# Performance work log

Hardware: AMD Instinct MI355X
Metric: run time of the kernel (lower is better)

## Reference

```python
import jax, jax.numpy as jnp
import numpy as np
import jax.scipy.linalg as jsl

K = 4           # num_hops + 1
N = 4096        # nodes
D = 256         # in_dim == out_dim
S = 32          # subspace_dim
ETA = 0.5
EPS = 0.5


def setup_inputs() -> dict:
    key = jax.random.key(0)
    k1, k2, k3 = jax.random.split(key, 3)
    hops = jax.random.normal(k1, (K, N, D), dtype=jnp.float32)
    A = (jax.random.uniform(k2, (N, N)) < 0.01).astype(jnp.float32)
    A = jnp.maximum(A, A.T)
    A = jnp.fill_diagonal(A, 1.0, inplace=False)
    deg = A.sum(axis=1)
    L = jnp.diag(deg) - A  # graph Laplacian
    # orthonormal subspace bases via QR, as in __init__
    raw = jax.random.normal(k3, (K, D, S), dtype=jnp.float32)
    q, _ = jnp.linalg.qr(raw)
    U = q[:, :, :S]
    hop_weights = jnp.ones((K,), dtype=jnp.float32) / K
    threshold = jnp.full((D,), 0.05, dtype=jnp.float32)
    lambda_lap = jnp.asarray(0.1, dtype=jnp.float32)
    return {"hops": hops, "adj_mask": A, "L": L, "U": U,
            "hop_weights": hop_weights, "threshold": threshold,
            "lambda_lap": lambda_lap}


def reference(hops, adj_mask, L, U, hop_weights, threshold, lambda_lap):
    n = hops.shape[1]
    s = U.shape[-1]
    w = jax.nn.softmax(hop_weights, axis=0)
    mask_add = (1.0 - adj_mask) * -1e9  # [n, n]
    I_s = jnp.eye(s, dtype=hops.dtype)
    agg_total = jnp.zeros((hops.shape[2], n), dtype=hops.dtype)  # [d, n]
    coeff = s / (n * EPS ** 2)
    for k in range(K):  # small fixed hop count
        Uk = U[k]                      # [d, s]
        Zk = Uk.T @ hops[k].T          # [s, n]
        M_k = I_s + coeff * (Zk @ Zk.T)  # [s, s]
        cf = jsl.cho_factor(M_k)
        M_inv = jsl.cho_solve(cf, I_s)   # Cholesky inverse
        MZ = M_inv @ Zk                  # [s, n]
        scores = Zk.T @ MZ + mask_add    # [n, n] Mahalanobis-style attention
        alpha = jax.nn.softmax(scores, axis=1)
        grad_k = Uk @ (MZ @ alpha.T)     # [d, n]
        agg_total = agg_total + w[k] * grad_k
    H_agg = agg_total.T                  # [n, d]
    lap_grad = lambda_lap * (L @ H_agg)
    H_half = hops[0] + ETA * H_agg - ETA * lap_grad
    # soft-threshold (proximal step); in_dim == out_dim so no proj
    H_out = jnp.sign(H_half) * jax.nn.relu(jnp.abs(H_half) - threshold[None, :])
    # orthogonality regularizer over subspace bases
    orth_loss = jnp.asarray(0.0, dtype=hops.dtype)
    for k in range(K):
        UkTUk = U[k].T @ U[k]
        orth_loss = orth_loss + ((UkTUk - I_s) ** 2).sum()
        for l in range(k + 1, K):
            orth_loss = orth_loss + ((U[k].T @ U[l]) ** 2).sum()
    lap_smooth = jnp.sum(H_out * (L @ H_out))  # trace(H^T L H)
    return (H_out, orth_loss, lap_smooth, jax.lax.stop_gradient(w))
```

## Files before the change

kernel.cpp:

```cpp
#include <hip/hip_runtime.h>
#include <cstddef>

typedef unsigned short ushortt;
typedef unsigned int uintt;

static constexpr int Nn = 4096;
static constexpr int Dd = 256;
static constexpr int Ss = 32;
static constexpr int Kk = 4;
static constexpr int ZBLK = 2048;
static constexpr int CAP = 128;
static constexpr int RST = 132;
static constexpr float kEta   = 0.5f;
static constexpr float kCoeff = 0.03125f;

__device__ __forceinline__ float waveReduceSum(float v){
  #pragma unroll
  for (int off = 32; off > 0; off >>= 1) v += __shfl_down(v, off, 64);
  return v;
}
__device__ __forceinline__ float blo(uintt u){ return __uint_as_float(u << 16); }
__device__ __forceinline__ float bhi(uintt u){ return __uint_as_float(u & 0xffff0000u); }
__device__ __forceinline__ ushortt f2b(float x){
  uintt u = __float_as_uint(x);
  uintt r = (u + 0x7fffu + ((u >> 16) & 1u)) >> 16;
  return (ushortt)r;
}
__device__ __forceinline__ float b2f(ushortt u){ return __uint_as_float(((uintt)u) << 16); }

__global__ __launch_bounds__(256) void buildz_kernel(const float* __restrict__ A,
                                                     const float* __restrict__ hw,
                                                     const float* __restrict__ hops,
                                                     const float* __restrict__ U,
                                                     int* __restrict__ deg,
                                                     int* __restrict__ colx,
                                                     float* __restrict__ Zt4,
                                                     float* __restrict__ Ubt,
                                                     float* __restrict__ out){
  int tid = threadIdx.x;
  if (blockIdx.x < ZBLK){
    int b = blockIdx.x;
    int k = b >> 9;
    int i0 = (b & 511) * 8;
    __shared__ float Us[32][132];
    int s = tid & 31, ii = tid >> 5;
    int i = i0 + ii;
    const float4* h4 = (const float4*)(hops + ((size_t)k * Nn + i) * Dd);
    float a0 = 0.f, a1 = 0.f, a2 = 0.f, a3 = 0.f;
    #pragma unroll
    for (int half = 0; half < 2; half++){
      if (half) __syncthreads();
      #pragma unroll
      for (int g = tid; g < 1024; g += 256){
        int d = g >> 3, s4 = (g & 7) * 4;
        float4 u = *(const float4*)(U + ((size_t)k * Dd + half * 128 + d) * Ss + s4);
        Us[s4 + 0][d] = u.x;
        Us[s4 + 1][d] = u.y;
        Us[s4 + 2][d] = u.z;
        Us[s4 + 3][d] = u.w;
      }
      __syncthreads();
      const float4* u4 = (const float4*)(&Us[s][0]);
      const float4* hh = h4 + half * 32;
      #pragma unroll 8
      for (int dq = 0; dq < 32; dq++){
        float4 h = hh[dq];
        float4 u = u4[dq];
        a0 = fmaf(h.x, u.x, a0);
        a1 = fmaf(h.y, u.y, a1);
        a2 = fmaf(h.z, u.z, a2);
        a3 = fmaf(h.w, u.w, a3);
      }
    }
    Zt4[(size_t)i * 128 + k * 32 + s] = (a0 + a1) + (a2 + a3);
    if (b < 128){
      int idx = b * 256 + tid;
      int c = idx >> 8, d = idx & 255;
      int kk = c >> 5, s2 = c & 31;
      Ubt[idx] = U[(size_t)kk * Dd * Ss + (size_t)d * Ss + s2];
    }
    return;
  }
  int i = blockIdx.x - ZBLK;
  if (i == 0 && tid == 0){
    out[1048576] = 0.f;
    out[1048577] = 0.f;
    float a0=hw[0], a1=hw[1], a2=hw[2], a3=hw[3];
    float mx = fmaxf(fmaxf(a0,a1), fmaxf(a2,a3));
    float e0=expf(a0-mx), e1=expf(a1-mx), e2=expf(a2-mx), e3=expf(a3-mx);
    float s = e0+e1+e2+e3;
    out[1048578]=e0/s; out[1048579]=e1/s; out[1048580]=e2/s; out[1048581]=e3/s;
  }
  int lane = tid & 63, w = tid >> 6;
  __shared__ int wbuf[4][96];
  __shared__ int wcnt[4];
  const float4* row4 = (const float4*)(A + (size_t)i * Nn);
  int cnt = 0;
  int base = w * 256;
  unsigned long long below = (lane == 63) ? 0x7fffffffffffffffull : ((1ull << lane) - 1ull);
  #pragma unroll
  for (int it = 0; it < 4; it++){
    int c4 = base + it * 64 + lane;
    float4 v = row4[c4];
    bool f0 = (v.x != 0.f), f1 = (v.y != 0.f), f2 = (v.z != 0.f), f3 = (v.w != 0.f);
    unsigned long long m0 = __ballot(f0), m1 = __ballot(f1),
                       m2 = __ballot(f2), m3 = __ballot(f3);
    int pre = __popcll(m0 & below) + __popcll(m1 & below)
            + __popcll(m2 & below) + __popcll(m3 & below);
    int pos = cnt + pre;
    int j0 = c4 * 4;
    if (f0){ if (pos < 96) wbuf[w][pos] = j0;     pos++; }
    if (f1){ if (pos < 96) wbuf[w][pos] = j0 + 1; pos++; }
    if (f2){ if (pos < 96) wbuf[w][pos] = j0 + 2; pos++; }
    if (f3){ if (pos < 96) wbuf[w][pos] = j0 + 3; pos++; }
    cnt += __popcll(m0) + __popcll(m1) + __popcll(m2) + __popcll(m3);
  }
  if (cnt > 96) cnt = 96;
  if (lane == 0) wcnt[w] = cnt;
  __syncthreads();
  int off = 0;
  for (int ww = 0; ww < w; ww++) off += wcnt[ww];
  int total = wcnt[0] + wcnt[1] + wcnt[2] + wcnt[3];
  for (int idx = lane; idx < cnt; idx += 64){
    int p = off + idx;
    if (p < CAP) colx[(size_t)i * CAP + p] = wbuf[w][idx];
  }
  if (tid == 0) deg[i] = (total < CAP) ? total : CAP;
}

__global__ __launch_bounds__(256) void mpart_kernel(const float* __restrict__ Zt4,
                                                    float* __restrict__ Mpart){
  int b = blockIdx.x;
  int k = b >> 4, ch = b & 15;
  int i0 = ch * 256;
  __shared__ float zs[256][33];
  for (int t = threadIdx.x; t < 256 * 32; t += 256){
    int ii = t >> 5, s = t & 31;
    zs[ii][s] = Zt4[(size_t)(i0 + ii) * 128 + k * 32 + s];
  }
  __syncthreads();
  int tid = threadIdx.x;
  int s2 = tid & 31, s1b = tid >> 5;
  float a0=0.f, a1=0.f, a2=0.f, a3=0.f;
  for (int ii = 0; ii < 256; ii++){
    float zc = zs[ii][s2];
    a0 = fmaf(zs[ii][s1b],      zc, a0);
    a1 = fmaf(zs[ii][8 + s1b],  zc, a1);
    a2 = fmaf(zs[ii][16 + s1b], zc, a2);
    a3 = fmaf(zs[ii][24 + s1b], zc, a3);
  }
  float* outp = Mpart + (size_t)b * 1024;
  outp[0 * 256 + tid] = a0;
  outp[1 * 256 + tid] = a1;
  outp[2 * 256 + tid] = a2;
  outp[3 * 256 + tid] = a3;
}

__global__ __launch_bounds__(256) void mzinv_kernel(const float* __restrict__ Zt4,
                                                    const float* __restrict__ Mpart,
                                                    ushortt* __restrict__ MZb){
  int b = blockIdx.x;
  int k = b >> 7;
  int i0 = (b & 127) * 32;
  __shared__ float mi[32][33];
  __shared__ float zs[32][33];
  int tid = threadIdx.x;
  for (int t = tid; t < 1024; t += 256){
    int ii = t >> 5, s2 = t & 31;
    zs[ii][s2] = Zt4[(size_t)(i0 + ii) * 128 + k * 32 + s2];
    float s = 0.f;
    #pragma unroll
    for (int ch = 0; ch < 16; ch++)
      s += Mpart[(size_t)(k * 16 + ch) * 1024 + t];
    mi[ii][s2] = kCoeff * s + ((ii == s2) ? 1.f : 0.f);
  }
  __syncthreads();
  if (tid < 64){
    int lane = tid, r = lane & 31, half = lane >> 5;
    float a[32];
    #pragma unroll
    for (int j = 0; j < 32; j++) a[j] = half ? ((r == j) ? 1.f : 0.f) : mi[r][j];
    #pragma unroll
    for (int p = 0; p < 32; p++){
      float app = __shfl(a[p], p, 64);
      float pinv = 1.f / app;
      float f = __shfl(a[p], r, 64);
      #pragma unroll
      for (int j = 0; j < 32; j++){
        float pr = __shfl(a[j], p + (half << 5), 64) * pinv;
        a[j] = (r == p) ? pr : fmaf(-f, pr, a[j]);
      }
    }
    if (half){
      #pragma unroll
      for (int j = 0; j < 32; j++) mi[r][j] = a[j];
    }
  }
  __syncthreads();
  int s = tid & 31;
  for (int rr = 0; rr < 4; rr++){
    int ii = rr * 8 + (tid >> 5);
    float acc = 0.f;
    #pragma unroll
    for (int s2 = 0; s2 < 32; s2++) acc = fmaf(mi[s][s2], zs[ii][s2], acc);
    MZb[(size_t)(i0 + ii) * 128 + k * 32 + s] = f2b(acc);
  }
}

__global__ __launch_bounds__(256) void agg_kernel(const float* __restrict__ Zt4,
                                                  const ushortt* __restrict__ MZb,
                                                  const float* __restrict__ wvec,
                                                  const int* __restrict__ deg,
                                                  const int* __restrict__ colx,
                                                  float* __restrict__ Vw){
  int i = blockIdx.x, tid = threadIdx.x;
  int lane = tid & 63, k = tid >> 6;
  __shared__ __align__(16) ushortt rows[CAP * RST];
  __shared__ int cols[CAP];
  __shared__ __align__(16) float zi[128];
  __shared__ float sc[4][CAP + 8];
  int m = deg[i];
  if (tid < 128) zi[tid] = Zt4[(size_t)i * 128 + tid];
  if (tid < m)  cols[tid] = colx[(size_t)i * CAP + tid];
  __syncthreads();

  int q = tid & 3, r = tid >> 2;
  float zq[32];
  {
    const float4* z4 = (const float4*)(&zi[q * 32]);
    #pragma unroll
    for (int p = 0; p < 8; p++){
      float4 z = z4[p];
      zq[p*4+0]=z.x; zq[p*4+1]=z.y; zq[p*4+2]=z.z; zq[p*4+3]=z.w;
    }
  }

  for (int t = r; t < m; t += 64){
    int j = cols[t];
    const uint4* src = (const uint4*)(MZb + (size_t)j * 128 + q * 32);
    uint4 q0 = src[0], q1 = src[1], q2 = src[2], q3 = src[3];
    uint4* dst = (uint4*)(rows + (size_t)t * RST + q * 32);
    dst[0] = q0; dst[1] = q1; dst[2] = q2; dst[3] = q3;
    float acc = 0.f;
    acc += blo(q0.x)*zq[0] + bhi(q0.x)*zq[1] + blo(q0.y)*zq[2] + bhi(q0.y)*zq[3];
    acc += blo(q0.z)*zq[4] + bhi(q0.z)*zq[5] + blo(q0.w)*zq[6] + bhi(q0.w)*zq[7];
    acc += blo(q1.x)*zq[8] + bhi(q1.x)*zq[9] + blo(q1.y)*zq[10]+ bhi(q1.y)*zq[11];
    acc += blo(q1.z)*zq[12]+ bhi(q1.z)*zq[13]+ blo(q1.w)*zq[14]+ bhi(q1.w)*zq[15];
    acc += blo(q2.x)*zq[16]+ bhi(q2.x)*zq[17]+ blo(q2.y)*zq[18]+ bhi(q2.y)*zq[19];
    acc += blo(q2.z)*zq[20]+ bhi(q2.z)*zq[21]+ blo(q2.w)*zq[22]+ bhi(q2.w)*zq[23];
    acc += blo(q3.x)*zq[24]+ bhi(q3.x)*zq[25]+ blo(q3.y)*zq[26]+ bhi(q3.y)*zq[27];
    acc += blo(q3.z)*zq[28]+ bhi(q3.z)*zq[29]+ blo(q3.w)*zq[30]+ bhi(q3.w)*zq[31];
    sc[q][t] = acc;
  }
  __syncthreads();

  float lmax = -3.0e38f;
  for (int t = lane; t < m; t += 64) lmax = fmaxf(lmax, sc[k][t]);
  #pragma unroll
  for (int off = 32; off > 0; off >>= 1) lmax = fmaxf(lmax, __shfl_xor(lmax, off, 64));
  float lsum = 0.f;
  for (int t = lane; t < m; t += 64){
    float e = __expf(sc[k][t] - lmax);
    sc[k][t] = e;
    lsum += e;
  }
  #pragma unroll
  for (int off = 32; off > 0; off >>= 1) lsum += __shfl_xor(lsum, off, 64);
  float scale = wvec[k] / lsum;

  int c2 = lane & 15, h = lane >> 4;
  float a0 = 0.f, a1 = 0.f;
  #pragma unroll 4
  for (int t = h; t < m; t += 4){
    uintt u = *(const uintt*)(rows + (size_t)t * RST + k * 32 + c2 * 2);
    float e = sc[k][t];
    a0 = fmaf(blo(u), e, a0);
    a1 = fmaf(bhi(u), e, a1);
  }
  a0 += __shfl_xor(a0, 16, 64); a0 += __shfl_xor(a0, 32, 64);
  a1 += __shfl_xor(a1, 16, 64); a1 += __shfl_xor(a1, 32, 64);
  if (h == 0){
    float2 v2 = make_float2(a0 * scale, a1 * scale);
    *(float2*)(Vw + (size_t)i * 128 + k * 32 + c2 * 2) = v2;
  }
}

__global__ __launch_bounds__(256) void gho_kernel(const float* __restrict__ Vw,
                                                  const float* __restrict__ Ubt,
                                                  const float* __restrict__ hops0,
                                                  const float* __restrict__ thr,
                                                  const float* __restrict__ U,
                                                  const float* __restrict__ lam_ptr,
                                                  const int* __restrict__ deg,
                                                  const int* __restrict__ colx,
                                                  float* __restrict__ out,
                                                  ushortt* __restrict__ Hb){
  int tid = threadIdx.x;
  if (blockIdx.x >= 1024){
    int g = (blockIdx.x - 1024) * 256 + tid;
    int pair = g >> 10;
    int idx = g & 1023;
    int s1 = idx >> 5, s2 = idx & 31;
    const int pk_[10] = {0,0,0,0,1,1,1,2,2,3};
    const int pl_[10] = {0,1,2,3,1,2,3,2,3,3};
    int pk = pk_[pair], pl = pl_[pair];
    const float* Uk = U + (size_t)pk * Dd * Ss;
    const float* Ul = U + (size_t)pl * Dd * Ss;
    float dot = 0.f;
    for (int d = 0; d < Dd; d++) dot += Uk[d * Ss + s1] * Ul[d * Ss + s2];
    float val = dot - ((pk == pl && s1 == s2) ? 1.f : 0.f);
    val *= val;
    val = waveReduceSum(val);
    __shared__ float redo[4];
    if ((tid & 63) == 0) redo[tid >> 6] = val;
    __syncthreads();
    if (tid == 0) atomicAdd(out + 1048576, redo[0] + redo[1] + redo[2] + redo[3]);
    return;
  }
  int i0 = blockIdx.x * 4;
  int lane = tid & 63, w = tid >> 6;
  __shared__ float Cs[4][132];
  __shared__ int cols_s[4][CAP];
  {
    int i = i0 + w;
    int m = deg[i];
    for (int t = lane; t < m; t += 64) cols_s[w][t] = colx[(size_t)i * CAP + t];
    float lam = lam_ptr[0];
    int half = lane >> 5, c32 = lane & 31;
    float4 acc = make_float4(0.f, 0.f, 0.f, 0.f);
    for (int t = half; t < m; t += 2){
      int j = cols_s[w][t];
      float4 v = ((const float4*)(Vw + (size_t)j * 128))[c32];
      acc.x += v.x; acc.y += v.y; acc.z += v.z; acc.w += v.w;
    }
    acc.x += __shfl_xor(acc.x, 32, 64);
    acc.y += __shfl_xor(acc.y, 32, 64);
    acc.z += __shfl_xor(acc.z, 32, 64);
    acc.w += __shfl_xor(acc.w, 32, 64);
    if (half == 0){
      float4 self = ((const float4*)(Vw + (size_t)i * 128))[c32];
      float ca = kEta * (1.f - lam * (float)m);
      float cb = kEta * lam;
      float4 o;
      o.x = fmaf(ca, self.x, cb * acc.x);
      o.y = fmaf(ca, self.y, cb * acc.y);
      o.z = fmaf(ca, self.z, cb * acc.z);
      o.w = fmaf(ca, self.w, cb * acc.w);
      *(float4*)(&Cs[w][c32 * 4]) = o;
    }
  }
  __syncthreads();
  int d4 = tid & 63, g = tid >> 6;
  float4 acc = make_float4(0.f, 0.f, 0.f, 0.f);
  #pragma unroll 4
  for (int c = 0; c < 128; c++){
    float4 ub = ((const float4*)(Ubt + (size_t)c * 256))[d4];
    float cs = Cs[g][c];
    acc.x = fmaf(cs, ub.x, acc.x);
    acc.y = fmaf(cs, ub.y, acc.y);
    acc.z = fmaf(cs, ub.z, acc.z);
    acc.w = fmaf(cs, ub.w, acc.w);
  }
  float4 th = ((const float4*)thr)[d4];
  int i = i0 + g;
  float4 hp = ((const float4*)(hops0 + (size_t)i * 256))[d4];
  float hx = hp.x + acc.x, hy = hp.y + acc.y;
  float hz = hp.z + acc.z, hw = hp.w + acc.w;
  float4 o;
  o.x = copysignf(fmaxf(fabsf(hx) - th.x, 0.f), hx);
  o.y = copysignf(fmaxf(fabsf(hy) - th.y, 0.f), hy);
  o.z = copysignf(fmaxf(fabsf(hz) - th.z, 0.f), hz);
  o.w = copysignf(fmaxf(fabsf(hw) - th.w, 0.f), hw);
  ((float4*)(out + (size_t)i * 256))[d4] = o;
  ushort4 hb;
  hb.x = f2b(o.x); hb.y = f2b(o.y); hb.z = f2b(o.z); hb.w = f2b(o.w);
  *((ushort4*)(Hb + (size_t)i * 256 + d4 * 4)) = hb;
}

__global__ __launch_bounds__(256) void lap_kernel(const float* __restrict__ Hout,
                                                  const ushortt* __restrict__ Hb,
                                                  const int* __restrict__ deg,
                                                  const int* __restrict__ colx,
                                                  float* __restrict__ lap_part){
  int i = blockIdx.x;
  int tid = threadIdx.x;
  int g = tid >> 7;
  int d2 = (tid & 127) * 2;
  __shared__ int cols[CAP];
  int m = deg[i];
  if (tid < m) cols[tid] = colx[(size_t)i * CAP + tid];
  __syncthreads();
  float nb0 = 0.f, nb1 = 0.f;
  #pragma unroll 8
  for (int t = g; t < m; t += 2){
    uintt u = *(const uintt*)(Hb + (size_t)cols[t] * 256 + d2);
    nb0 += blo(u);
    nb1 += bhi(u);
  }
  float2 hv = *(const float2*)(Hout + (size_t)i * 256 + d2);
  float part = -hv.x * nb0 - hv.y * nb1;
  if (g == 0) part += (float)m * (hv.x * hv.x + hv.y * hv.y);
  part = waveReduceSum(part);
  __shared__ float red[4];
  if ((tid & 63) == 0) red[tid >> 6] = part;
  __syncthreads();
  if (tid == 0) lap_part[i] = red[0] + red[1] + red[2] + red[3];
}

__global__ __launch_bounds__(256) void lapred_kernel(const float* __restrict__ lap_part,
                                                     float* __restrict__ out){
  int tid = threadIdx.x;
  float s = 0.f;
  const float4* p4 = (const float4*)lap_part;
  #pragma unroll
  for (int q = 0; q < 4; q++){
    float4 v = p4[q * 256 + tid];
    s += v.x + v.y + v.z + v.w;
  }
  s = waveReduceSum(s);
  __shared__ float red[4];
  if ((tid & 63) == 0) red[tid >> 6] = s;
  __syncthreads();
  if (tid == 0) out[1048577] = red[0] + red[1] + red[2] + red[3];
}

extern "C" void kernel_launch(void* const* d_in, const int* in_sizes, int n_in,
                              void* d_out, int out_size, void* d_ws, size_t ws_size,
                              hipStream_t stream)
{
  const float* hops = (const float*)d_in[0];
  const float* A    = (const float*)d_in[1];
  const float* L    = (const float*)d_in[2];
  const float* U    = (const float*)d_in[3];
  const float* hw   = (const float*)d_in[4];
  const float* thr  = (const float*)d_in[5];
  const float* lam  = (const float*)d_in[6];
  (void)L; (void)in_sizes; (void)n_in; (void)out_size; (void)ws_size;

  float* out = (float*)d_out;
  float* ws  = (float*)d_ws;

  float*   Zt4   = ws;
  float*   Vw    = ws + 524288;
  float*   Mpart = ws + 1048576;
  ushortt* MZb   = (ushortt*)(ws + 1572864);
  ushortt* Hb    = (ushortt*)(ws + 1835008);
  float*   Ubt   = ws + 2359296;
  int*     deg   = (int*)(ws + 2461696);
  int*     colx  = (int*)(ws + 2465792);
  float*   lapp  = ws + 3121152;

  float* w_out = out + 1048578;

  buildz_kernel<<<Nn + ZBLK, 256, 0, stream>>>(A, hw, hops, U, deg, colx, Zt4, Ubt, out);
  mpart_kernel <<<Kk*16, 256, 0, stream>>>(Zt4, Mpart);
  mzinv_kernel <<<Kk*128, 256, 0, stream>>>(Zt4, Mpart, MZb);
  agg_kernel   <<<Nn, 256, 0, stream>>>(Zt4, MZb, w_out, deg, colx, Vw);
  gho_kernel   <<<1064, 256, 0, stream>>>(Vw, Ubt, hops, thr, U, lam, deg, colx, out, Hb);
  lap_kernel   <<<Nn, 256, 0, stream>>>(out, Hb, deg, colx, lapp);
  lapred_kernel<<<1, 256, 0, stream>>>(lapp, out);
}
```

Before: 285.3 us.

## Split attention aggregation into one block per node and hop

New measurement: 286.6 us. About the same (+0.5%).

```diff
diff --git a/kernel.cpp b/kernel.cpp
--- a/kernel.cpp
+++ b/kernel.cpp
@@ -10,7 +10,6 @@
 static constexpr int Kk = 4;
 static constexpr int ZBLK = 2048;
 static constexpr int CAP = 128;
-static constexpr int RST = 132;
 static constexpr float kEta   = 0.5f;
 static constexpr float kCoeff = 0.03125f;
 
@@ -213,75 +212,77 @@
                                                   const int* __restrict__ deg,
                                                   const int* __restrict__ colx,
                                                   float* __restrict__ Vw){
-  int i = blockIdx.x, tid = threadIdx.x;
-  int lane = tid & 63, k = tid >> 6;
-  __shared__ __align__(16) ushortt rows[CAP * RST];
+  int b = blockIdx.x;
+  int i = b >> 2, k = b & 3;
+  int tid = threadIdx.x;
+  __shared__ __align__(16) ushortt rows[CAP][40];
   __shared__ int cols[CAP];
-  __shared__ __align__(16) float zi[128];
-  __shared__ float sc[4][CAP + 8];
+  __shared__ float sc[CAP + 8];
+  __shared__ float zsh[32];
+  __shared__ float red[4][16][2];
+  __shared__ float scale_sh;
   int m = deg[i];
-  if (tid < 128) zi[tid] = Zt4[(size_t)i * 128 + tid];
   if (tid < m)  cols[tid] = colx[(size_t)i * CAP + tid];
-  __syncthreads();
-
-  int q = tid & 3, r = tid >> 2;
-  float zq[32];
-  {
-    const float4* z4 = (const float4*)(&zi[q * 32]);
-    #pragma unroll
-    for (int p = 0; p < 8; p++){
-      float4 z = z4[p];
-      zq[p*4+0]=z.x; zq[p*4+1]=z.y; zq[p*4+2]=z.z; zq[p*4+3]=z.w;
-    }
-  }
-
-  for (int t = r; t < m; t += 64){
-    int j = cols[t];
-    const uint4* src = (const uint4*)(MZb + (size_t)j * 128 + q * 32);
+  if (tid < 32) zsh[tid] = Zt4[(size_t)i * 128 + k * 32 + tid];
+  __syncthreads();
+
+  if (tid < m){
+    int j = cols[tid];
+    const uint4* src = (const uint4*)(MZb + (size_t)j * 128 + k * 32);
     uint4 q0 = src[0], q1 = src[1], q2 = src[2], q3 = src[3];
-    uint4* dst = (uint4*)(rows + (size_t)t * RST + q * 32);
-    dst[0] = q0; dst[1] = q1; dst[2] = q2; dst[3] = q3;
+    *(uint4*)(&rows[tid][0])  = q0;
+    *(uint4*)(&rows[tid][8])  = q1;
+    *(uint4*)(&rows[tid][16]) = q2;
+    *(uint4*)(&rows[tid][24]) = q3;
     float acc = 0.f;
-    acc += blo(q0.x)*zq[0] + bhi(q0.x)*zq[1] + blo(q0.y)*zq[2] + bhi(q0.y)*zq[3];
-    acc += blo(q0.z)*zq[4] + bhi(q0.z)*zq[5] + blo(q0.w)*zq[6] + bhi(q0.w)*zq[7];
-    acc += blo(q1.x)*zq[8] + bhi(q1.x)*zq[9] + blo(q1.y)*zq[10]+ bhi(q1.y)*zq[11];
-    acc += blo(q1.z)*zq[12]+ bhi(q1.z)*zq[13]+ blo(q1.w)*zq[14]+ bhi(q1.w)*zq[15];
-    acc += blo(q2.x)*zq[16]+ bhi(q2.x)*zq[17]+ blo(q2.y)*zq[18]+ bhi(q2.y)*zq[19];
-    acc += blo(q2.z)*zq[20]+ bhi(q2.z)*zq[21]+ blo(q2.w)*zq[22]+ bhi(q2.w)*zq[23];
-    acc += blo(q3.x)*zq[24]+ bhi(q3.x)*zq[25]+ blo(q3.y)*zq[26]+ bhi(q3.y)*zq[27];
-    acc += blo(q3.z)*zq[28]+ bhi(q3.z)*zq[29]+ blo(q3.w)*zq[30]+ bhi(q3.w)*zq[31];
-    sc[q][t] = acc;
-  }
-  __syncthreads();
-
-  float lmax = -3.0e38f;
-  for (int t = lane; t < m; t += 64) lmax = fmaxf(lmax, sc[k][t]);
-  #pragma unroll
-  for (int off = 32; off > 0; off >>= 1) lmax = fmaxf(lmax, __shfl_xor(lmax, off, 64));
-  float lsum = 0.f;
-  for (int t = lane; t < m; t += 64){
-    float e = __expf(sc[k][t] - lmax);
-    sc[k][t] = e;
-    lsum += e;
-  }
-  #pragma unroll
-  for (int off = 32; off > 0; off >>= 1) lsum += __shfl_xor(lsum, off, 64);
-  float scale = wvec[k] / lsum;
-
-  int c2 = lane & 15, h = lane >> 4;
+    acc += blo(q0.x)*zsh[0] + bhi(q0.x)*zsh[1] + blo(q0.y)*zsh[2] + bhi(q0.y)*zsh[3];
+    acc += blo(q0.z)*zsh[4] + bhi(q0.z)*zsh[5] + blo(q0.w)*zsh[6] + bhi(q0.w)*zsh[7];
+    acc += blo(q1.x)*zsh[8] + bhi(q1.x)*zsh[9] + blo(q1.y)*zsh[10]+ bhi(q1.y)*zsh[11];
+    acc += blo(q1.z)*zsh[12]+ bhi(q1.z)*zsh[13]+ blo(q1.w)*zsh[14]+ bhi(q1.w)*zsh[15];
+    acc += blo(q2.x)*zsh[16]+ bhi(q2.x)*zsh[17]+ blo(q2.y)*zsh[18]+ bhi(q2.y)*zsh[19];
+    acc += blo(q2.z)*zsh[20]+ bhi(q2.z)*zsh[21]+ blo(q2.w)*zsh[22]+ bhi(q2.w)*zsh[23];
+    acc += blo(q3.x)*zsh[24]+ bhi(q3.x)*zsh[25]+ blo(q3.y)*zsh[26]+ bhi(q3.y)*zsh[27];
+    acc += blo(q3.z)*zsh[28]+ bhi(q3.z)*zsh[29]+ blo(q3.w)*zsh[30]+ bhi(q3.w)*zsh[31];
+    sc[tid] = acc;
+  }
+  __syncthreads();
+
+  if (tid < 64){
+    int lane = tid;
+    float lmax = -3.0e38f;
+    for (int t = lane; t < m; t += 64) lmax = fmaxf(lmax, sc[t]);
+    #pragma unroll
+    for (int off = 32; off > 0; off >>= 1) lmax = fmaxf(lmax, __shfl_xor(lmax, off, 64));
+    float lsum = 0.f;
+    for (int t = lane; t < m; t += 64){
+      float e = __expf(sc[t] - lmax);
+      sc[t] = e;
+      lsum += e;
+    }
+    #pragma unroll
+    for (int off = 32; off > 0; off >>= 1) lsum += __shfl_xor(lsum, off, 64);
+    if (lane == 0) scale_sh = wvec[k] / lsum;
+  }
+  __syncthreads();
+  float scale = scale_sh;
+
+  int c2 = tid & 15, h = tid >> 4;
   float a0 = 0.f, a1 = 0.f;
-  #pragma unroll 4
-  for (int t = h; t < m; t += 4){
-    uintt u = *(const uintt*)(rows + (size_t)t * RST + k * 32 + c2 * 2);
-    float e = sc[k][t];
+  for (int t = h; t < m; t += 16){
+    uintt u = *(const uintt*)(&rows[t][c2 * 2]);
+    float e = sc[t];
     a0 = fmaf(blo(u), e, a0);
     a1 = fmaf(bhi(u), e, a1);
   }
   a0 += __shfl_xor(a0, 16, 64); a0 += __shfl_xor(a0, 32, 64);
   a1 += __shfl_xor(a1, 16, 64); a1 += __shfl_xor(a1, 32, 64);
-  if (h == 0){
-    float2 v2 = make_float2(a0 * scale, a1 * scale);
-    *(float2*)(Vw + (size_t)i * 128 + k * 32 + c2 * 2) = v2;
+  int w = tid >> 6, lane = tid & 63;
+  if ((lane >> 4) == 0){ red[w][c2][0] = a0; red[w][c2][1] = a1; }
+  __syncthreads();
+  if (tid < 16){
+    float s0 = red[0][tid][0] + red[1][tid][0] + red[2][tid][0] + red[3][tid][0];
+    float s1 = red[0][tid][1] + red[1][tid][1] + red[2][tid][1] + red[3][tid][1];
+    *(float2*)(Vw + (size_t)i * 128 + k * 32 + tid * 2) = make_float2(s0 * scale, s1 * scale);
   }
 }
 
@@ -455,7 +456,7 @@
   buildz_kernel<<<Nn + ZBLK, 256, 0, stream>>>(A, hw, hops, U, deg, colx, Zt4, Ubt, out);
   mpart_kernel <<<Kk*16, 256, 0, stream>>>(Zt4, Mpart);
   mzinv_kernel <<<Kk*128, 256, 0, stream>>>(Zt4, Mpart, MZb);
-  agg_kernel   <<<Nn, 256, 0, stream>>>(Zt4, MZb, w_out, deg, colx, Vw);
+  agg_kernel   <<<4*Nn, 256, 0, stream>>>(Zt4, MZb, w_out, deg, colx, Vw);
   gho_kernel   <<<1064, 256, 0, stream>>>(Vw, Ubt, hops, thr, U, lam, deg, colx, out, Hb);
   lap_kernel   <<<Nn, 256, 0, stream>>>(out, Hb, deg, colx, lapp);
   lapred_kernel<<<1, 256, 0, stream>>>(lapp, out);
```

## Split gho rows across two waves each and reuse Ubt loads across rows

Applied to the files above, without the earlier changes.

Result: no change. 281.4 us (-1.4%).

```diff
diff --git a/kernel.cpp b/kernel.cpp
--- a/kernel.cpp
+++ b/kernel.cpp
@@ -296,8 +296,8 @@
                                                   float* __restrict__ out,
                                                   ushortt* __restrict__ Hb){
   int tid = threadIdx.x;
-  if (blockIdx.x >= 1024){
-    int g = (blockIdx.x - 1024) * 256 + tid;
+  if (blockIdx.x >= 2048){
+    int g = (blockIdx.x - 2048) * 256 + tid;
     int pair = g >> 10;
     int idx = g & 1023;
     int s1 = idx >> 5, s2 = idx & 31;
@@ -317,19 +317,22 @@
     if (tid == 0) atomicAdd(out + 1048576, redo[0] + redo[1] + redo[2] + redo[3]);
     return;
   }
-  int i0 = blockIdx.x * 4;
+  int i0 = blockIdx.x * 2;
   int lane = tid & 63, w = tid >> 6;
-  __shared__ float Cs[4][132];
-  __shared__ int cols_s[4][CAP];
+  __shared__ float Cs[2][132];
+  __shared__ int cols_s[2][CAP];
+  __shared__ __align__(16) float4 Pac[2][4][64];
   {
-    int i = i0 + w;
+    int r = w >> 1, p = w & 1;
+    int i = i0 + r;
     int m = deg[i];
-    for (int t = lane; t < m; t += 64) cols_s[w][t] = colx[(size_t)i * CAP + t];
-    float lam = lam_ptr[0];
+    int t0 = p * 64 + lane;
+    if (t0 < m) cols_s[r][t0] = colx[(size_t)i * CAP + t0];
+    __syncthreads();
     int half = lane >> 5, c32 = lane & 31;
     float4 acc = make_float4(0.f, 0.f, 0.f, 0.f);
-    for (int t = half; t < m; t += 2){
-      int j = cols_s[w][t];
+    for (int t = p * 2 + half; t < m; t += 4){
+      int j = cols_s[r][t];
       float4 v = ((const float4*)(Vw + (size_t)j * 128))[c32];
       acc.x += v.x; acc.y += v.y; acc.z += v.z; acc.w += v.w;
     }
@@ -337,44 +340,68 @@
     acc.y += __shfl_xor(acc.y, 32, 64);
     acc.z += __shfl_xor(acc.z, 32, 64);
     acc.w += __shfl_xor(acc.w, 32, 64);
-    if (half == 0){
-      float4 self = ((const float4*)(Vw + (size_t)i * 128))[c32];
-      float ca = kEta * (1.f - lam * (float)m);
-      float cb = kEta * lam;
-      float4 o;
-      o.x = fmaf(ca, self.x, cb * acc.x);
-      o.y = fmaf(ca, self.y, cb * acc.y);
-      o.z = fmaf(ca, self.z, cb * acc.z);
-      o.w = fmaf(ca, self.w, cb * acc.w);
-      *(float4*)(&Cs[w][c32 * 4]) = o;
-    }
-  }
-  __syncthreads();
-  int d4 = tid & 63, g = tid >> 6;
-  float4 acc = make_float4(0.f, 0.f, 0.f, 0.f);
-  #pragma unroll 4
-  for (int c = 0; c < 128; c++){
-    float4 ub = ((const float4*)(Ubt + (size_t)c * 256))[d4];
-    float cs = Cs[g][c];
-    acc.x = fmaf(cs, ub.x, acc.x);
-    acc.y = fmaf(cs, ub.y, acc.y);
-    acc.z = fmaf(cs, ub.z, acc.z);
-    acc.w = fmaf(cs, ub.w, acc.w);
-  }
-  float4 th = ((const float4*)thr)[d4];
-  int i = i0 + g;
-  float4 hp = ((const float4*)(hops0 + (size_t)i * 256))[d4];
-  float hx = hp.x + acc.x, hy = hp.y + acc.y;
-  float hz = hp.z + acc.z, hw = hp.w + acc.w;
-  float4 o;
-  o.x = copysignf(fmaxf(fabsf(hx) - th.x, 0.f), hx);
-  o.y = copysignf(fmaxf(fabsf(hy) - th.y, 0.f), hy);
-  o.z = copysignf(fmaxf(fabsf(hz) - th.z, 0.f), hz);
-  o.w = copysignf(fmaxf(fabsf(hw) - th.w, 0.f), hw);
-  ((float4*)(out + (size_t)i * 256))[d4] = o;
-  ushort4 hb;
-  hb.x = f2b(o.x); hb.y = f2b(o.y); hb.z = f2b(o.z); hb.w = f2b(o.w);
-  *((ushort4*)(Hb + (size_t)i * 256 + d4 * 4)) = hb;
+    if (half == 0) Pac[r][p][c32] = acc;
+  }
+  __syncthreads();
+  if (tid < 64){
+    int r = tid >> 5, c32 = tid & 31;
+    int i = i0 + r;
+    int m = deg[i];
+    float lam = lam_ptr[0];
+    float4 p0 = Pac[r][0][c32];
+    float4 p1 = Pac[r][1][c32];
+    float4 self = ((const float4*)(Vw + (size_t)i * 128))[c32];
+    float ca = kEta * (1.f - lam * (float)m);
+    float cb = kEta * lam;
+    float4 o;
+    o.x = fmaf(ca, self.x, cb * (p0.x + p1.x));
+    o.y = fmaf(ca, self.y, cb * (p0.y + p1.y));
+    o.z = fmaf(ca, self.z, cb * (p0.z + p1.z));
+    o.w = fmaf(ca, self.w, cb * (p0.w + p1.w));
+    *(float4*)(&Cs[r][c32 * 4]) = o;
+  }
+  __syncthreads();
+  int d4 = tid & 63, cs = tid >> 6;
+  {
+    float4 f0 = make_float4(0.f, 0.f, 0.f, 0.f);
+    float4 f1 = make_float4(0.f, 0.f, 0.f, 0.f);
+    int cbase = cs * 32;
+    #pragma unroll 4
+    for (int c = cbase; c < cbase + 32; c++){
+      float4 ub = ((const float4*)(Ubt + (size_t)c * 256))[d4];
+      float c0 = Cs[0][c], c1 = Cs[1][c];
+      f0.x = fmaf(c0, ub.x, f0.x); f0.y = fmaf(c0, ub.y, f0.y);
+      f0.z = fmaf(c0, ub.z, f0.z); f0.w = fmaf(c0, ub.w, f0.w);
+      f1.x = fmaf(c1, ub.x, f1.x); f1.y = fmaf(c1, ub.y, f1.y);
+      f1.z = fmaf(c1, ub.z, f1.z); f1.w = fmaf(c1, ub.w, f1.w);
+    }
+    Pac[0][cs][d4] = f0;
+    Pac[1][cs][d4] = f1;
+  }
+  __syncthreads();
+  if (tid < 128){
+    int r = tid >> 6;
+    int i = i0 + r;
+    float4 pa = Pac[r][0][d4], pb = Pac[r][1][d4], pc = Pac[r][2][d4], pd = Pac[r][3][d4];
+    float4 acc;
+    acc.x = (pa.x + pb.x) + (pc.x + pd.x);
+    acc.y = (pa.y + pb.y) + (pc.y + pd.y);
+    acc.z = (pa.z + pb.z) + (pc.z + pd.z);
+    acc.w = (pa.w + pb.w) + (pc.w + pd.w);
+    float4 th = ((const float4*)thr)[d4];
+    float4 hp = ((const float4*)(hops0 + (size_t)i * 256))[d4];
+    float hx = hp.x + acc.x, hy = hp.y + acc.y;
+    float hz = hp.z + acc.z, hw = hp.w + acc.w;
+    float4 o;
+    o.x = copysignf(fmaxf(fabsf(hx) - th.x, 0.f), hx);
+    o.y = copysignf(fmaxf(fabsf(hy) - th.y, 0.f), hy);
+    o.z = copysignf(fmaxf(fabsf(hz) - th.z, 0.f), hz);
+    o.w = copysignf(fmaxf(fabsf(hw) - th.w, 0.f), hw);
+    ((float4*)(out + (size_t)i * 256))[d4] = o;
+    ushort4 hb;
+    hb.x = f2b(o.x); hb.y = f2b(o.y); hb.z = f2b(o.z); hb.w = f2b(o.w);
+    *((ushort4*)(Hb + (size_t)i * 256 + d4 * 4)) = hb;
+  }
 }
 
 __global__ __launch_bounds__(256) void lap_kernel(const float* __restrict__ Hout,
@@ -456,7 +483,7 @@
   mpart_kernel <<<Kk*16, 256, 0, stream>>>(Zt4, Mpart);
   mzinv_kernel <<<Kk*128, 256, 0, stream>>>(Zt4, Mpart, MZb);
   agg_kernel   <<<Nn, 256, 0, stream>>>(Zt4, MZb, w_out, deg, colx, Vw);
-  gho_kernel   <<<1064, 256, 0, stream>>>(Vw, Ubt, hops, thr, U, lam, deg, colx, out, Hb);
+  gho_kernel   <<<2088, 256, 0, stream>>>(Vw, Ubt, hops, thr, U, lam, deg, colx, out, Hb);
   lap_kernel   <<<Nn, 256, 0, stream>>>(out, Hb, deg, colx, lapp);
   lapred_kernel<<<1, 256, 0, stream>>>(lapp, out);
 }
```
